# Optimization experiments

Measured on AMD Instinct MI355X. Metric: run time of the kernel, lower is better.

Reference implementation:

```python
import jax, jax.numpy as jnp
import numpy as np

B, L, S, H, D, P = 2, 1024, 1024, 8, 64, 4  # n_params = n_qubits * n_layers = 4


def setup_inputs() -> dict:
    key = jax.random.key(0)
    ks = jax.random.split(key, 7)
    w_scale = 1.0 / np.sqrt(D)  # ~Linear default init scale
    return {
        "queries": jax.random.normal(ks[0], (B, L, H, D), dtype=jnp.float32),
        "keys":    jax.random.normal(ks[1], (B, S, H, D), dtype=jnp.float32),
        "values":  jax.random.normal(ks[2], (B, S, H, D), dtype=jnp.float32),
        "Wq": jax.random.normal(ks[3], (D, P), dtype=jnp.float32) * w_scale,
        "bq": jnp.zeros((P,), dtype=jnp.float32),
        "Wk": jax.random.normal(ks[4], (D, P), dtype=jnp.float32) * w_scale,
        "bk": jnp.zeros((P,), dtype=jnp.float32),
    }


def reference(queries, keys, values, Wq, bq, Wk, bk):
    # queries: [B,L,H,D], keys/values: [B,S,H,D]
    head_dim = queries.shape[-1]
    pi = jnp.float32(np.pi)

    # Angle projections (tanh-squashed to [-pi, pi])
    q_params = jnp.tanh(queries @ Wq + bq) * pi  # [B,L,H,P]
    k_params = jnp.tanh(keys @ Wk + bk) * pi     # [B,S,H,P]

    qp = q_params.transpose(0, 2, 1, 3)  # [B,H,L,P]
    kp = k_params.transpose(0, 2, 1, 3)  # [B,H,S,P]

    # Hadamard test expval = Re<psi(k)|psi(q)>. For a single RY layer followed
    # by a CNOT ring (which cancels in the overlap), this equals
    # prod_i cos((q_i - k_i)/2)  -- exact closed form of the QNode output.
    half_diff = 0.5 * (qp[:, :, :, None, :] - kp[:, :, None, :, :])  # [B,H,L,S,P]
    scores = jnp.prod(jnp.cos(half_diff), axis=-1)                   # [B,H,L,S]
    scores = scores / jnp.sqrt(jnp.float32(head_dim))

    attn_weights = jax.nn.softmax(scores, axis=-1)  # [B,H,L,S]
    # dropout is identity in eval mode

    v = values.transpose(0, 2, 1, 3)                       # [B,H,S,D]
    context = jnp.einsum("bhls,bhsd->blhd", attn_weights, v)  # [B,L,H,D]
    return context, attn_weights
```

## Files before the change

### kernel.cpp

```cpp
#include <hip/hip_runtime.h>
#include <math.h>

#define BB 2
#define LL 1024
#define SS 1024
#define HH 8
#define DD 64
#define PP 4
#define TL 16

typedef __attribute__((ext_vector_type(8))) short short8;
typedef __attribute__((ext_vector_type(4))) float floatx4;

#if __has_builtin(__builtin_amdgcn_cosf)
#define COS2PI(x) __builtin_amdgcn_cosf(x)
#else
#define COS2PI(x) __cosf((x) * 6.283185307179586f)
#endif
#if __has_builtin(__builtin_amdgcn_exp2f)
#define EXP2F(x) __builtin_amdgcn_exp2f(x)
#else
#define EXP2F(x) exp2f(x)
#endif

__device__ __forceinline__ float scoreP(float4 q, float k0, float k1, float k2, float k3) {
    float c0 = COS2PI(q.x - k0);
    float c1 = COS2PI(q.y - k1);
    float c2 = COS2PI(q.z - k2);
    float c3 = COS2PI(q.w - k3);
    float prod = (c0 * c1) * (c2 * c3);
    return EXP2F(prod * 0.18033688011112042f);
}

__device__ __forceinline__ unsigned f2bf(float f) {
    unsigned u = __float_as_uint(f);
    u += 0x7FFF + ((u >> 16) & 1);
    return u >> 16;
}
__device__ __forceinline__ float bf2f(unsigned u) { return __uint_as_float(u << 16); }

__global__ __launch_bounds__(256) void qka_prep_kernel(
    const float* __restrict__ Q, const float* __restrict__ K, const float* __restrict__ V,
    const float* __restrict__ Wq, const float* __restrict__ bq,
    const float* __restrict__ Wk, const float* __restrict__ bk,
    float* __restrict__ qp_ws, float* __restrict__ kp_ws, unsigned short* __restrict__ vt_ws)
{
    __shared__ float vt[64 * 66];
    const int bid = blockIdx.x;
    const int t = threadIdx.x;

    if (bid < 8192) {
        const int wid  = (bid * 256 + t) >> 6;
        const int lane = t & 63;
        const int NQ = BB * LL * HH;
        const bool is_q = (wid < NQ);
        const int r = is_q ? wid : wid - NQ;
        const int b   = r >> 13;
        const int rem = r & 8191;
        const int l   = rem >> 3;
        const int h   = rem & 7;

        const float* in   = is_q ? Q  : K;
        const float* W    = is_q ? Wq : Wk;
        const float* bias = is_q ? bq : bk;

        float x = in[(size_t)r * DD + lane];
        float4 w = *reinterpret_cast<const float4*>(W + lane * PP);
        float p0 = x * w.x, p1 = x * w.y, p2 = x * w.z, p3 = x * w.w;
        #pragma unroll
        for (int off = 1; off < 64; off <<= 1) {
            p0 += __shfl_xor(p0, off);
            p1 += __shfl_xor(p1, off);
            p2 += __shfl_xor(p2, off);
            p3 += __shfl_xor(p3, off);
        }
        if (lane < PP) {
            float s = (lane == 0) ? p0 : (lane == 1) ? p1 : (lane == 2) ? p2 : p3;
            float v = 0.25f * tanhf(s + bias[lane]);
            float* outp = is_q ? qp_ws : kp_ws;
            outp[(((size_t)(b * HH + h)) * LL + l) * PP + lane] = v;
        }
    } else {
        const int tile = bid - 8192;
        const int b  = tile >> 7;
        const int h  = (tile >> 4) & 7;
        const int s0 = (tile & 15) * 64;
        const int bh = b * HH + h;

        #pragma unroll
        for (int i = 0; i < 4; ++i) {
            int n = i * 256 + t;
            int s = n >> 4, dq = n & 15;
            float4 v = *reinterpret_cast<const float4*>(
                V + (((size_t)(b * SS + s0 + s)) * HH + h) * DD + dq * 4);
            vt[(dq * 4 + 0) * 66 + s] = v.x;
            vt[(dq * 4 + 1) * 66 + s] = v.y;
            vt[(dq * 4 + 2) * 66 + s] = v.z;
            vt[(dq * 4 + 3) * 66 + s] = v.w;
        }
        __syncthreads();
        unsigned* outp = reinterpret_cast<unsigned*>(vt_ws);
        #pragma unroll
        for (int rr = 0; rr < 8; ++rr) {
            int idx = rr * 256 + t;
            int d = idx >> 5, sp = idx & 31;
            float a = vt[d * 66 + 2 * sp];
            float c = vt[d * 66 + 2 * sp + 1];
            unsigned pk = f2bf(a) | (f2bf(c) << 16);
            outp[((size_t)bh * DD + d) * (SS / 2) + (s0 >> 1) + sp] = pk;
        }
    }
}

__global__ __launch_bounds__(256) void qka_main_kernel(
    const float* __restrict__ qp_ws,
    const float* __restrict__ kp_ws,
    const unsigned short* __restrict__ vt_ws,
    float* __restrict__ out_ctx,
    float* __restrict__ out_attn)
{
    __shared__ unsigned short kp[SS * PP];
    __shared__ unsigned short Pm[TL * SS];

    const int t   = threadIdx.x;
    const int bid = blockIdx.x;
    const int lt  = bid & 63;
    const int h   = (bid >> 6) & 7;
    const int b   = bid >> 9;
    const int bh  = b * HH + h;

    const float4* kps = reinterpret_cast<const float4*>(kp_ws + (size_t)bh * SS * PP);
    #pragma unroll
    for (int r = 0; r < 4; ++r) {
        int s = r * 256 + t;
        float4 kv = kps[s];
        uint2 pk;
        pk.x = f2bf(kv.x) | (f2bf(kv.y) << 16);
        pk.y = f2bf(kv.z) | (f2bf(kv.w) << 16);
        *reinterpret_cast<uint2*>(&kp[s * 4]) = pk;
    }
    __syncthreads();

    const int wv = t >> 6, lane = t & 63;
    const int r0 = wv * 4;

    float4 q4[4];
    #pragma unroll
    for (int i = 0; i < 4; ++i)
        q4[i] = *reinterpret_cast<const float4*>(
            qp_ws + ((size_t)bh * LL + lt * TL + r0 + i) * PP);

    float zacc[4] = {0.f, 0.f, 0.f, 0.f};
    for (int c = 0; c < 8; ++c) {
        int s = c * 128 + lane * 2;
        uint4 kk = *reinterpret_cast<const uint4*>(&kp[s * 4]);
        float ka0 = bf2f(kk.x & 0xffffu), ka1 = bf2f(kk.x >> 16);
        float ka2 = bf2f(kk.y & 0xffffu), ka3 = bf2f(kk.y >> 16);
        float kb0 = bf2f(kk.z & 0xffffu), kb1 = bf2f(kk.z >> 16);
        float kb2 = bf2f(kk.w & 0xffffu), kb3 = bf2f(kk.w >> 16);
        #pragma unroll
        for (int i = 0; i < 4; ++i) {
            float e0 = scoreP(q4[i], ka0, ka1, ka2, ka3);
            float e1 = scoreP(q4[i], kb0, kb1, kb2, kb3);
            zacc[i] += e0 + e1;
            unsigned pk = f2bf(e0) | (f2bf(e1) << 16);
            int row = r0 + i;
            unsigned byte = (unsigned)(row * 2048 + c * 256 + lane * 4) ^ ((row & 7) << 4);
            *reinterpret_cast<unsigned*>(reinterpret_cast<char*>(Pm) + byte) = pk;
        }
    }

    #pragma unroll
    for (int i = 0; i < 4; ++i) {
        float z = zacc[i];
        #pragma unroll
        for (int off = 1; off < 64; off <<= 1) z += __shfl_xor(z, off);
        zacc[i] = 1.0f / z;
    }

    #pragma unroll
    for (int i = 0; i < 4; ++i) {
        int row = r0 + i;
        float rz = zacc[i];
        unsigned sw = (row & 7) << 4;
        float* abase = out_attn + ((size_t)bh * LL + lt * TL + row) * SS;
        #pragma unroll
        for (int it = 0; it < 4; ++it) {
            unsigned byte = (unsigned)(row * 2048 + it * 512 + lane * 8) ^ sw;
            uint2 pk = *reinterpret_cast<uint2*>(reinterpret_cast<char*>(Pm) + byte);
            float w0 = bf2f(pk.x & 0xffffu) * rz, w1 = bf2f(pk.x >> 16) * rz;
            float w2 = bf2f(pk.y & 0xffffu) * rz, w3 = bf2f(pk.y >> 16) * rz;
            floatx4 wv4 = {w0, w1, w2, w3};
            __builtin_nontemporal_store(wv4,
                reinterpret_cast<floatx4*>(abase + it * 256 + lane * 4));
            uint2 wb;
            wb.x = f2bf(w0) | (f2bf(w1) << 16);
            wb.y = f2bf(w2) | (f2bf(w3) << 16);
            *reinterpret_cast<uint2*>(reinterpret_cast<char*>(Pm) + byte) = wb;
        }
    }
    __syncthreads();

    const int d0 = wv * 16;
    const int fr = lane & 15;
    const int hi = lane >> 4;
    floatx4 acc = {0.f, 0.f, 0.f, 0.f};
    const unsigned short* vtb = vt_ws + ((size_t)bh * DD + d0 + fr) * SS + hi * 8;
    const unsigned swf = (unsigned)((fr & 7) << 4);
    #pragma unroll 4
    for (int st = 0; st < 32; ++st) {
        unsigned abyte = (unsigned)(fr * 2048 + st * 64 + hi * 16) ^ swf;
        short8 afrag = *reinterpret_cast<const short8*>(
            reinterpret_cast<char*>(Pm) + abyte);
        short8 bfrag = *reinterpret_cast<const short8*>(vtb + st * 32);
        acc = __builtin_amdgcn_mfma_f32_16x16x32_bf16(afrag, bfrag, acc, 0, 0, 0);
    }
    #pragma unroll
    for (int r = 0; r < 4; ++r) {
        int l = lt * TL + hi * 4 + r;
        __builtin_nontemporal_store(acc[r],
            out_ctx + (((size_t)b * LL + l) * HH + h) * DD + d0 + fr);
    }
}

extern "C" void kernel_launch(void* const* d_in, const int* in_sizes, int n_in,
                              void* d_out, int out_size, void* d_ws, size_t ws_size,
                              hipStream_t stream) {
    const float* Q  = (const float*)d_in[0];
    const float* K  = (const float*)d_in[1];
    const float* V  = (const float*)d_in[2];
    const float* Wq = (const float*)d_in[3];
    const float* bq = (const float*)d_in[4];
    const float* Wk = (const float*)d_in[5];
    const float* bk = (const float*)d_in[6];

    float* out_ctx  = (float*)d_out;
    float* out_attn = out_ctx + (size_t)BB * LL * HH * DD;

    float* qp_ws = (float*)d_ws;
    float* kp_ws = qp_ws + (size_t)BB * HH * LL * PP;
    unsigned short* vt_ws = (unsigned short*)(kp_ws + (size_t)BB * HH * SS * PP);

    qka_prep_kernel<<<8448, 256, 0, stream>>>(Q, K, V, Wq, bq, Wk, bk, qp_ws, kp_ws, vt_ws);

    qka_main_kernel<<<BB * HH * (LL / TL), 256, 0, stream>>>(
        qp_ws, kp_ws, vt_ws, out_ctx, out_attn);
}
```

Before: 43.20 us.

## Tile Q/K projection through LDS, use hardware bf16 pack, keep scores in registers

The prep kernel now has each block load a 64-row tile of Q or K into shared memory and compute all four projections per thread. This replaces the per-row wavefront shuffle reductions and cuts the grid from 8448 to 768 blocks. Software bf16 rounding is replaced with the v_cvt_pk_bf16_f32 instruction. The main kernel keeps the packed exp scores in registers instead of round-tripping them through LDS before normalization, and adds an occupancy hint to launch bounds. The costs are more register pressure and narrower 8-byte attention stores in place of 16-byte ones.

```diff
diff --git a/kernel.cpp b/kernel.cpp
--- a/kernel.cpp
+++ b/kernel.cpp
@@ -11,6 +11,7 @@
 
 typedef __attribute__((ext_vector_type(8))) short short8;
 typedef __attribute__((ext_vector_type(4))) float floatx4;
+typedef __attribute__((ext_vector_type(2))) float floatx2;
 
 #if __has_builtin(__builtin_amdgcn_cosf)
 #define COS2PI(x) __builtin_amdgcn_cosf(x)
@@ -32,10 +33,10 @@
     return EXP2F(prod * 0.18033688011112042f);
 }
 
-__device__ __forceinline__ unsigned f2bf(float f) {
-    unsigned u = __float_as_uint(f);
-    u += 0x7FFF + ((u >> 16) & 1);
-    return u >> 16;
+__device__ __forceinline__ unsigned cvt_pk_bf16(float a, float b) {
+    unsigned r;
+    asm("v_cvt_pk_bf16_f32 %0, %1, %2" : "=v"(r) : "v"(a), "v"(b));
+    return r;
 }
 __device__ __forceinline__ float bf2f(unsigned u) { return __uint_as_float(u << 16); }
 
@@ -45,47 +46,54 @@
     const float* __restrict__ Wk, const float* __restrict__ bk,
     float* __restrict__ qp_ws, float* __restrict__ kp_ws, unsigned short* __restrict__ vt_ws)
 {
-    __shared__ float vt[64 * 66];
+    __shared__ float sm[4480];
     const int bid = blockIdx.x;
     const int t = threadIdx.x;
 
-    if (bid < 8192) {
-        const int wid  = (bid * 256 + t) >> 6;
-        const int lane = t & 63;
-        const int NQ = BB * LL * HH;
-        const bool is_q = (wid < NQ);
-        const int r = is_q ? wid : wid - NQ;
-        const int b   = r >> 13;
-        const int rem = r & 8191;
-        const int l   = rem >> 3;
-        const int h   = rem & 7;
-
+    if (bid < 512) {
+        const bool is_q = (bid < 256);
+        const int r_base = (is_q ? bid : bid - 256) * 64;
         const float* in   = is_q ? Q  : K;
         const float* W    = is_q ? Wq : Wk;
         const float* bias = is_q ? bq : bk;
 
-        float x = in[(size_t)r * DD + lane];
-        float4 w = *reinterpret_cast<const float4*>(W + lane * PP);
-        float p0 = x * w.x, p1 = x * w.y, p2 = x * w.z, p3 = x * w.w;
-        #pragma unroll
-        for (int off = 1; off < 64; off <<= 1) {
-            p0 += __shfl_xor(p0, off);
-            p1 += __shfl_xor(p1, off);
-            p2 += __shfl_xor(p2, off);
-            p3 += __shfl_xor(p3, off);
-        }
-        if (lane < PP) {
-            float s = (lane == 0) ? p0 : (lane == 1) ? p1 : (lane == 2) ? p2 : p3;
-            float v = 0.25f * tanhf(s + bias[lane]);
-            float* outp = is_q ? qp_ws : kp_ws;
-            outp[(((size_t)(b * HH + h)) * LL + l) * PP + lane] = v;
-        }
+        float* tile = sm;
+        float* Wl   = sm + 64 * 65;
+
+        #pragma unroll
+        for (int i = 0; i < 4; ++i) {
+            int n = i * 256 + t;
+            int row = n >> 4, dq = n & 15;
+            float4 v = *reinterpret_cast<const float4*>(in + ((size_t)(r_base + row)) * DD + dq * 4);
+            tile[row * 65 + dq * 4 + 0] = v.x;
+            tile[row * 65 + dq * 4 + 1] = v.y;
+            tile[row * 65 + dq * 4 + 2] = v.z;
+            tile[row * 65 + dq * 4 + 3] = v.w;
+        }
+        Wl[t] = W[t];
+        __syncthreads();
+
+        const int row = t & 63;
+        const int p   = t >> 6;
+        float acc = 0.f;
+        #pragma unroll 16
+        for (int d = 0; d < DD; ++d)
+            acc += tile[row * 65 + d] * Wl[d * PP + p];
+
+        const int r = r_base + row;
+        const int b   = r >> 13;
+        const int l   = (r & 8191) >> 3;
+        const int h   = r & 7;
+        float v = 0.25f * tanhf(acc + bias[p]);
+        float* outp = is_q ? qp_ws : kp_ws;
+        outp[(((size_t)(b * HH + h)) * LL + l) * PP + p] = v;
     } else {
-        const int tile = bid - 8192;
-        const int b  = tile >> 7;
-        const int h  = (tile >> 4) & 7;
-        const int s0 = (tile & 15) * 64;
+        const int tile_i = bid - 512;
+        const int b  = tile_i >> 7;
+        const int h  = (tile_i >> 4) & 7;
+        const int s0 = (tile_i & 15) * 64;
         const int bh = b * HH + h;
+        float* vt = sm;
 
         #pragma unroll
         for (int i = 0; i < 4; ++i) {
@@ -104,15 +112,13 @@
         for (int rr = 0; rr < 8; ++rr) {
             int idx = rr * 256 + t;
             int d = idx >> 5, sp = idx & 31;
-            float a = vt[d * 66 + 2 * sp];
-            float c = vt[d * 66 + 2 * sp + 1];
-            unsigned pk = f2bf(a) | (f2bf(c) << 16);
+            unsigned pk = cvt_pk_bf16(vt[d * 66 + 2 * sp], vt[d * 66 + 2 * sp + 1]);
             outp[((size_t)bh * DD + d) * (SS / 2) + (s0 >> 1) + sp] = pk;
         }
     }
 }
 
-__global__ __launch_bounds__(256) void qka_main_kernel(
+__global__ __launch_bounds__(256, 4) void qka_main_kernel(
     const float* __restrict__ qp_ws,
     const float* __restrict__ kp_ws,
     const unsigned short* __restrict__ vt_ws,
@@ -135,8 +141,8 @@
         int s = r * 256 + t;
         float4 kv = kps[s];
         uint2 pk;
-        pk.x = f2bf(kv.x) | (f2bf(kv.y) << 16);
-        pk.y = f2bf(kv.z) | (f2bf(kv.w) << 16);
+        pk.x = cvt_pk_bf16(kv.x, kv.y);
+        pk.y = cvt_pk_bf16(kv.z, kv.w);
         *reinterpret_cast<uint2*>(&kp[s * 4]) = pk;
     }
     __syncthreads();
@@ -150,7 +156,9 @@
         q4[i] = *reinterpret_cast<const float4*>(
             qp_ws + ((size_t)bh * LL + lt * TL + r0 + i) * PP);
 
+    unsigned pk[4][8];
     float zacc[4] = {0.f, 0.f, 0.f, 0.f};
+    #pragma unroll
     for (int c = 0; c < 8; ++c) {
         int s = c * 128 + lane * 2;
         uint4 kk = *reinterpret_cast<const uint4*>(&kp[s * 4]);
@@ -163,10 +171,7 @@
             float e0 = scoreP(q4[i], ka0, ka1, ka2, ka3);
             float e1 = scoreP(q4[i], kb0, kb1, kb2, kb3);
             zacc[i] += e0 + e1;
-            unsigned pk = f2bf(e0) | (f2bf(e1) << 16);
-            int row = r0 + i;
-            unsigned byte = (unsigned)(row * 2048 + c * 256 + lane * 4) ^ ((row & 7) << 4);
-            *reinterpret_cast<unsigned*>(reinterpret_cast<char*>(Pm) + byte) = pk;
+            pk[i][c] = cvt_pk_bf16(e0, e1);
         }
     }
 
@@ -183,20 +188,16 @@
         int row = r0 + i;
         float rz = zacc[i];
         unsigned sw = (row & 7) << 4;
-        float* abase = out_attn + ((size_t)bh * LL + lt * TL + row) * SS;
-        #pragma unroll
-        for (int it = 0; it < 4; ++it) {
-            unsigned byte = (unsigned)(row * 2048 + it * 512 + lane * 8) ^ sw;
-            uint2 pk = *reinterpret_cast<uint2*>(reinterpret_cast<char*>(Pm) + byte);
-            float w0 = bf2f(pk.x & 0xffffu) * rz, w1 = bf2f(pk.x >> 16) * rz;
-            float w2 = bf2f(pk.y & 0xffffu) * rz, w3 = bf2f(pk.y >> 16) * rz;
-            floatx4 wv4 = {w0, w1, w2, w3};
-            __builtin_nontemporal_store(wv4,
-                reinterpret_cast<floatx4*>(abase + it * 256 + lane * 4));
-            uint2 wb;
-            wb.x = f2bf(w0) | (f2bf(w1) << 16);
-            wb.y = f2bf(w2) | (f2bf(w3) << 16);
-            *reinterpret_cast<uint2*>(reinterpret_cast<char*>(Pm) + byte) = wb;
+        float* abase = out_attn + ((size_t)bh * LL + lt * TL + row) * SS + lane * 2;
+        #pragma unroll
+        for (int c = 0; c < 8; ++c) {
+            unsigned p = pk[i][c];
+            float w0 = bf2f(p & 0xffffu) * rz;
+            float w1 = bf2f(p >> 16) * rz;
+            floatx2 wv2 = {w0, w1};
+            __builtin_nontemporal_store(wv2, reinterpret_cast<floatx2*>(abase + c * 128));
+            unsigned byte = (unsigned)(row * 2048 + c * 256 + lane * 4) ^ sw;
+            *reinterpret_cast<unsigned*>(reinterpret_cast<char*>(Pm) + byte) = cvt_pk_bf16(w0, w1);
         }
     }
     __syncthreads();
@@ -241,7 +242,7 @@
     float* kp_ws = qp_ws + (size_t)BB * HH * LL * PP;
     unsigned short* vt_ws = (unsigned short*)(kp_ws + (size_t)BB * HH * SS * PP);
 
-    qka_prep_kernel<<<8448, 256, 0, stream>>>(Q, K, V, Wq, bq, Wk, bk, qp_ws, kp_ws, vt_ws);
+    qka_prep_kernel<<<768, 256, 0, stream>>>(Q, K, V, Wq, bq, Wk, bk, qp_ws, kp_ws, vt_ws);
 
     qka_main_kernel<<<BB * HH * (LL / TL), 256, 0, stream>>>(
         qp_ws, kp_ws, vt_ws, out_ctx, out_attn);
```

Result: faster. 35.45 us (median of 2 runs) (-17.9%).
